# Kernel optimization log

Measured on AMD Instinct MI355X. Metric: run time of the kernel, lower is better.

## Reference

```python
import jax, jax.numpy as jnp
import numpy as np

B, C_IN, C_OUT, N, L = 4, 128, 256, 4096, 4
D = C_OUT // 4
EPS_BN = 1e-5


def setup_inputs() -> dict:
    key = jax.random.key(0)
    ks = jax.random.split(key, 16)
    s_in = 1.0 / np.sqrt(C_IN)
    s_out = 1.0 / np.sqrt(C_OUT)
    return {
        "features": jax.random.normal(ks[0], (B, C_IN, N), dtype=jnp.float32),
        # LBR: conv1x1 -> BN -> ReLU -> conv1x1 -> BN -> ReLU
        "lbr_w1": jax.random.uniform(ks[1], (C_OUT, C_IN), jnp.float32, -s_in, s_in),
        "lbr_g1": jnp.ones((C_OUT,), jnp.float32),
        "lbr_b1": jnp.zeros((C_OUT,), jnp.float32),
        "lbr_w2": jax.random.uniform(ks[2], (C_OUT, C_OUT), jnp.float32, -s_out, s_out),
        "lbr_g2": jnp.ones((C_OUT,), jnp.float32),
        "lbr_b2": jnp.zeros((C_OUT,), jnp.float32),
        # per-layer OffsetAttention params (stacked on leading L axis)
        # q_conv and k_conv share the same weight (q_conv.weight = k_conv.weight)
        "attn_qk_w": jax.random.uniform(ks[3], (L, D, C_OUT), jnp.float32, -s_out, s_out),
        "attn_v_w": jax.random.uniform(ks[4], (L, C_OUT, C_OUT), jnp.float32, -s_out, s_out),
        "attn_v_b": jax.random.uniform(ks[5], (L, C_OUT), jnp.float32, -s_out, s_out),
        "attn_t_w": jax.random.uniform(ks[6], (L, C_OUT, C_OUT), jnp.float32, -s_out, s_out),
        "attn_t_b": jax.random.uniform(ks[7], (L, C_OUT), jnp.float32, -s_out, s_out),
        "attn_bn_g": jnp.ones((L, C_OUT), jnp.float32),
        "attn_bn_b": jnp.zeros((L, C_OUT), jnp.float32),
    }


def batchnorm1d(x, gamma, beta):
    # x: [B, C, N]; training-mode BN: batch stats over (B, N), biased variance
    mean = jnp.mean(x, axis=(0, 2), keepdims=True)
    var = jnp.mean(jnp.square(x - mean), axis=(0, 2), keepdims=True)
    xn = (x - mean) * jax.lax.rsqrt(var + EPS_BN)
    return xn * gamma[None, :, None] + beta[None, :, None]


def offset_attention(x, qk_w, v_w, v_b, t_w, t_b, bn_g, bn_b):
    # x: [B, C, N]
    K = jnp.einsum("dc,bcn->bdn", qk_w, x)            # [B, D, N]
    # Q = same conv, permuted to [B, N, D]; attention_map = Q @ K -> [B, N, N]
    attn = jnp.einsum("bdn,bdm->bnm", K, K)
    attn = jax.nn.softmax(attn, axis=-1)
    # extra L1 renorm over dim=1 (column-wise)
    attn = attn / (1e-9 + jnp.sum(attn, axis=1, keepdims=True))
    V = jnp.einsum("dc,bcn->bdn", v_w, x) + v_b[None, :, None]  # [B, C, N]
    new_feat = jnp.einsum("bcn,bnm->bcm", V, attn)    # [B, C, N]
    off = x - new_feat
    t = jnp.einsum("dc,bcn->bdn", t_w, off) + t_b[None, :, None]
    return jax.nn.relu(batchnorm1d(t, bn_g, bn_b))


def reference(features, lbr_w1, lbr_g1, lbr_b1, lbr_w2, lbr_g2, lbr_b2,
              attn_qk_w, attn_v_w, attn_v_b, attn_t_w, attn_t_b,
              attn_bn_g, attn_bn_b):
    # LBR stem
    h = jnp.einsum("dc,bcn->bdn", lbr_w1, features)
    h = jax.nn.relu(batchnorm1d(h, lbr_g1, lbr_b1))
    h = jnp.einsum("dc,bcn->bdn", lbr_w2, h)
    h = jax.nn.relu(batchnorm1d(h, lbr_g2, lbr_b2))
    # stacked offset attention; output concatenates attention outputs only
    outs = []
    cur = h
    for i in range(L):
        cur = offset_attention(cur, attn_qk_w[i], attn_v_w[i], attn_v_b[i],
                               attn_t_w[i], attn_t_b[i], attn_bn_g[i], attn_bn_b[i])
        outs.append(cur)
    return jnp.concatenate(outs, axis=1)  # [B, C_OUT*L, N]
```

## Files before the change

### kernel.cpp

```cpp
#include <hip/hip_runtime.h>
#include <hip/hip_bf16.h>
#include <math.h>

#define NPTS 4096
#define CO   256
#define CI   128
#define BB   4
#define DQ   64
#define LL   4
#define PST  136

typedef __attribute__((ext_vector_type(8))) short bf16x8;
typedef __attribute__((ext_vector_type(4))) float f32x4;

#define MFMA16(a,b,c) __builtin_amdgcn_mfma_f32_16x16x32_bf16((a),(b),(c),0,0,0)

__device__ __forceinline__ short fb(float x) {
  __hip_bfloat16 h = __float2bfloat16(x);
  return __builtin_bit_cast(short, h);
}
__device__ __forceinline__ float bf(short s) {
  unsigned u = ((unsigned)(unsigned short)s) << 16;
  return __builtin_bit_cast(float, u);
}

__global__ __launch_bounds__(256) void cvt5_k(
    const float* __restrict__ s1, short* __restrict__ d1, int n1,
    const float* __restrict__ s2, short* __restrict__ d2, int n2,
    const float* __restrict__ s3, short* __restrict__ d3, int n3,
    const float* __restrict__ s4, short* __restrict__ d4, int n4,
    const float* __restrict__ s5, short* __restrict__ d5, int n5)
{
  int i = blockIdx.x * 256 + threadIdx.x;
  const float* S; short* D;
  if      (i < n1)                       { S = s1; D = d1; }
  else if ((i -= n1) < n2)               { S = s2; D = d2; }
  else if ((i -= n2) < n3)               { S = s3; D = d3; }
  else if ((i -= n3) < n4)               { S = s4; D = d4; }
  else if ((i -= n4) < n5)               { S = s5; D = d5; }
  else return;
  const float4 a = ((const float4*)S)[i * 2];
  const float4 b = ((const float4*)S)[i * 2 + 1];
  bf16x8 r;
  r[0] = fb(a.x); r[1] = fb(a.y); r[2] = fb(a.z); r[3] = fb(a.w);
  r[4] = fb(b.x); r[5] = fb(b.y); r[6] = fb(b.z); r[7] = fb(b.w);
  ((bf16x8*)D)[i] = r;
}

__global__ __launch_bounds__(256) void tcvt_k(
    const float* __restrict__ X, long xbs, int C, short* __restrict__ XT)
{
  const int n0 = blockIdx.x * 64, c0 = blockIdx.y * 64, b = blockIdx.z;
  const int t = threadIdx.x, tl = t & 63, tg = t >> 6;
  __shared__ float xs[64][65];
#pragma unroll
  for (int r = 0; r < 16; ++r) {
    const int cc = tg * 16 + r;
    xs[cc][tl] = X[(long)b * xbs + (long)(c0 + cc) * NPTS + n0 + tl];
  }
  __syncthreads();
#pragma unroll
  for (int r = 0; r < 16; ++r) {
    const int nn = tg * 16 + r;
    XT[((long)b * NPTS + n0 + nn) * C + c0 + tl] = fb(xs[tl][nn]);
  }
}

template<int OMODE, bool BIAS>
__global__ __launch_bounds__(256) void conv_a(
    const short* __restrict__ XT, int C,
    const short* __restrict__ Wb, const float* __restrict__ bias,
    short* __restrict__ Yv, long ybs,
    float* __restrict__ ps1, float* __restrict__ ps2)
{
  const int n0 = blockIdx.x * 64, d0 = blockIdx.y * 64, b = blockIdx.z;
  const int tid = threadIdx.x, w = tid >> 6, l = tid & 63, lg = l >> 4, lr = l & 15;
  const short* xb = XT + (long)b * NPTS * C;
  f32x4 acc[4];
#pragma unroll
  for (int i = 0; i < 4; ++i) acc[i] = (f32x4){0.f, 0.f, 0.f, 0.f};
  const int dr = d0 + w * 16 + lr;
  for (int kc = 0; kc < C; kc += 32) {
    const bf16x8 af = *(const bf16x8*)&Wb[(long)dr * C + kc + lg * 8];
#pragma unroll
    for (int ni = 0; ni < 4; ++ni) {
      const bf16x8 bx = *(const bf16x8*)&xb[(long)(n0 + ni * 16 + lr) * C + kc + lg * 8];
      acc[ni] = MFMA16(af, bx, acc[ni]);
    }
  }
  float bv[4] = {0.f, 0.f, 0.f, 0.f};
  if (BIAS) {
    const float4 b4 = *(const float4*)&bias[d0 + w * 16 + lg * 4];
    bv[0] = b4.x; bv[1] = b4.y; bv[2] = b4.z; bv[3] = b4.w;
  }
  const int db = d0 + w * 16 + lg * 4;
  float s1[4], s2[4];
#pragma unroll
  for (int j = 0; j < 4; ++j) { s1[j] = 0.f; s2[j] = 0.f; }
#pragma unroll
  for (int ni = 0; ni < 4; ++ni) {
    const int n = n0 + ni * 16 + lr;
#pragma unroll
    for (int j = 0; j < 4; ++j) {
      const short ob = fb(acc[ni][j] + bv[j]);
      if constexpr (OMODE == 1) {
        Yv[(long)b * ybs + ((long)(n >> 7) * CO + db + j) * 128 + (n & 127)] = ob;
      } else {
        Yv[(long)b * ybs + (long)(db + j) * NPTS + n] = ob;
        const float o = bf(ob);
        s1[j] += o; s2[j] += o * o;
      }
    }
  }
  if constexpr (OMODE == 2) {
#pragma unroll
    for (int j = 0; j < 4; ++j) {
#pragma unroll
      for (int off = 1; off < 16; off <<= 1) {
        s1[j] += __shfl_xor(s1[j], off);
        s2[j] += __shfl_xor(s2[j], off);
      }
    }
    if (lr == 0) {
      const int slot = b * 64 + blockIdx.x;
#pragma unroll
      for (int j = 0; j < 4; ++j) {
        ps1[(long)(db + j) * 256 + slot] = s1[j];
        ps2[(long)(db + j) * 256 + slot] = s2[j];
      }
    }
  }
}

__global__ __launch_bounds__(256) void conv_b(
    const short* __restrict__ XT, const short* __restrict__ Wb,
    short* __restrict__ KTo)
{
  const int n0 = blockIdx.x * 64, b = blockIdx.y;
  const int tid = threadIdx.x, w = tid >> 6, l = tid & 63, lg = l >> 4, lr = l & 15;
  const short* xb = XT + (long)b * NPTS * CO;
  f32x4 acc[4];
#pragma unroll
  for (int i = 0; i < 4; ++i) acc[i] = (f32x4){0.f, 0.f, 0.f, 0.f};
  const long nr = n0 + w * 16 + lr;
  for (int kc = 0; kc < CO; kc += 32) {
    const bf16x8 af = *(const bf16x8*)&xb[nr * CO + kc + lg * 8];
#pragma unroll
    for (int di = 0; di < 4; ++di) {
      const bf16x8 wf = *(const bf16x8*)&Wb[(long)(di * 16 + lr) * CO + kc + lg * 8];
      acc[di] = MFMA16(af, wf, acc[di]);
    }
  }
  short* Ko = KTo + (long)b * NPTS * DQ;
  const int nb = n0 + w * 16 + lg * 4;
#pragma unroll
  for (int j = 0; j < 4; ++j) {
#pragma unroll
    for (int di = 0; di < 4; ++di)
      Ko[(long)(nb + j) * DQ + di * 16 + lr] = fb(acc[di][j]);
  }
}

__global__ __launch_bounds__(64) void bnfin_k(
    const float* __restrict__ ps1, const float* __restrict__ ps2,
    float* __restrict__ mean, float* __restrict__ rstd)
{
  const int c = blockIdx.x, t = threadIdx.x;
  float s = 0.f, s2 = 0.f;
#pragma unroll
  for (int i = 0; i < 4; ++i) {
    s  += ps1[(long)c * 256 + t + i * 64];
    s2 += ps2[(long)c * 256 + t + i * 64];
  }
#pragma unroll
  for (int o = 32; o > 0; o >>= 1) { s += __shfl_down(s, o); s2 += __shfl_down(s2, o); }
  if (t == 0) {
    const float m = s / (float)(BB * NPTS);
    const float v = s2 / (float)(BB * NPTS) - m * m;
    mean[c] = m;
    rstd[c] = rsqrtf(v + 1e-5f);
  }
}

template<bool WF32, bool WBF>
__global__ __launch_bounds__(256) void bnrelu_t(
    const short* __restrict__ X, long xbs,
    const float* __restrict__ mean, const float* __restrict__ rstd,
    const float* __restrict__ g, const float* __restrict__ be,
    float* __restrict__ Yf, long ybs, short* __restrict__ XT)
{
  const int n0 = blockIdx.x * 64, c0 = blockIdx.y * 64, b = blockIdx.z;
  const int t = threadIdx.x, tl = t & 63, tg = t >> 6;
  __shared__ float xs[64][65];
#pragma unroll
  for (int r = 0; r < 16; ++r) {
    const int cc = tg * 16 + r, c = c0 + cc;
    float v = bf(X[(long)b * xbs + (long)c * NPTS + n0 + tl]);
    v = fmaxf((v - mean[c]) * rstd[c] * g[c] + be[c], 0.f);
    if (WF32) Yf[(long)b * ybs + (long)c * NPTS + n0 + tl] = v;
    xs[cc][tl] = v;
  }
  __syncthreads();
  if (WBF) {
#pragma unroll
    for (int r = 0; r < 16; ++r) {
      const int nn = tg * 16 + r;
      XT[((long)b * NPTS + n0 + nn) * CO + c0 + tl] = fb(xs[tl][nn]);
    }
  }
}

__global__ __launch_bounds__(256) void rowstats_mfma(
    const short* __restrict__ KT, float* __restrict__ pmax, float* __restrict__ psum)
{
  const int bid = blockIdx.x;
  const int b = (bid >> 1) & 3;
  const int idx = (bid >> 3) * 2 + (bid & 1);
  const int n0 = (idx & 63) * 64;
  const int chunk = idx >> 6;
  const int tid = threadIdx.x, w = tid >> 6, l = tid & 63, lg = l >> 4, lr = l & 15;
  const short* Kb = KT + (long)b * NPTS * DQ;
  const int nr = n0 + w * 16 + lr;
  const bf16x8 a0 = *(const bf16x8*)&Kb[(long)nr * DQ + lg * 8];
  const bf16x8 a1 = *(const bf16x8*)&Kb[(long)nr * DQ + 32 + lg * 8];
  const int mc = chunk * (NPTS / 4);

  float mx[4][4];
#pragma unroll
  for (int p = 0; p < 4; ++p)
#pragma unroll
    for (int j = 0; j < 4; ++j) mx[p][j] = -INFINITY;
  for (int m0 = mc; m0 < mc + NPTS / 4; m0 += 64) {
#pragma unroll
    for (int p = 0; p < 4; ++p) {
      const bf16x8 b0 = *(const bf16x8*)&Kb[(long)(m0 + p * 16 + lr) * DQ + lg * 8];
      const bf16x8 b1 = *(const bf16x8*)&Kb[(long)(m0 + p * 16 + lr) * DQ + 32 + lg * 8];
      f32x4 s = {0.f, 0.f, 0.f, 0.f};
      s = MFMA16(a0, b0, s);
      s = MFMA16(a1, b1, s);
#pragma unroll
      for (int j = 0; j < 4; ++j) mx[p][j] = fmaxf(mx[p][j], s[j]);
    }
  }
  float mxf[4];
#pragma unroll
  for (int j = 0; j < 4; ++j)
    mxf[j] = fmaxf(fmaxf(mx[0][j], mx[1][j]), fmaxf(mx[2][j], mx[3][j]));
#pragma unroll
  for (int off = 1; off < 16; off <<= 1)
#pragma unroll
    for (int j = 0; j < 4; ++j) mxf[j] = fmaxf(mxf[j], __shfl_xor(mxf[j], off));

  float sm[4] = {0.f, 0.f, 0.f, 0.f};
  for (int m0 = mc; m0 < mc + NPTS / 4; m0 += 64) {
#pragma unroll
    for (int p = 0; p < 4; ++p) {
      const bf16x8 b0 = *(const bf16x8*)&Kb[(long)(m0 + p * 16 + lr) * DQ + lg * 8];
      const bf16x8 b1 = *(const bf16x8*)&Kb[(long)(m0 + p * 16 + lr) * DQ + 32 + lg * 8];
      f32x4 s = {0.f, 0.f, 0.f, 0.f};
      s = MFMA16(a0, b0, s);
      s = MFMA16(a1, b1, s);
#pragma unroll
      for (int j = 0; j < 4; ++j) sm[j] += __expf(s[j] - mxf[j]);
    }
  }
#pragma unroll
  for (int off = 1; off < 16; off <<= 1)
#pragma unroll
    for (int j = 0; j < 4; ++j) sm[j] += __shfl_xor(sm[j], off);

  if (lr == 0) {
    const long base = ((long)chunk * BB + b) * NPTS + n0 + w * 16 + lg * 4;
#pragma unroll
    for (int j = 0; j < 4; ++j) { pmax[base + j] = mxf[j]; psum[base + j] = sm[j]; }
  }
}

__global__ __launch_bounds__(256) void combine_k(
    const float* __restrict__ pmax, const float* __restrict__ psum,
    float* __restrict__ rmax, float* __restrict__ rinv)
{
  const long i = (long)blockIdx.x * 256 + threadIdx.x;
  const long st = (long)BB * NPTS;
  float m = pmax[i];
  m = fmaxf(m, pmax[st + i]); m = fmaxf(m, pmax[2 * st + i]); m = fmaxf(m, pmax[3 * st + i]);
  const float s = psum[i] * __expf(pmax[i] - m)
                + psum[st + i] * __expf(pmax[st + i] - m)
                + psum[2 * st + i] * __expf(pmax[2 * st + i] - m)
                + psum[3 * st + i] * __expf(pmax[3 * st + i] - m);
  rmax[i] = m;
  rinv[i] = 1.f / s;
}

__global__ __launch_bounds__(512) void pass2_mfma(
    const short* __restrict__ KT, const short* __restrict__ Vblk,
    const float* __restrict__ rmax, const float* __restrict__ rinv,
    short* __restrict__ XO)
{
  const int bid = blockIdx.x;
  const int b  = (bid >> 1) & 3;
  const int m0 = ((bid >> 3) * 2 + (bid & 1)) * 64;
  const int tid = threadIdx.x;
  const int w = tid >> 6, l = tid & 63, lg = l >> 4, lr = l & 15;

  const short* Kb = KT + (long)b * NPTS * DQ;
  const short* Vb = Vblk + (long)b * CO * NPTS;
  const float* rmb = rmax + (long)b * NPTS;
  const float* rib = rinv + (long)b * NPTS;

  __shared__ short Ps[2][64][PST];
  __shared__ float cspart[8][64];
  __shared__ float csum[64];

  bf16x8 bK[4][2];
#pragma unroll
  for (int ms = 0; ms < 4; ++ms) {
    bK[ms][0] = *(const bf16x8*)&Kb[(long)(m0 + ms * 16 + lr) * DQ + lg * 8];
    bK[ms][1] = *(const bf16x8*)&Kb[(long)(m0 + ms * 16 + lr) * DQ + 32 + lg * 8];
  }

  f32x4 acc[4][2];
#pragma unroll
  for (int i = 0; i < 4; ++i) {
    acc[i][0] = (f32x4){0.f, 0.f, 0.f, 0.f};
    acc[i][1] = (f32x4){0.f, 0.f, 0.f, 0.f};
  }
  float cs[4] = {0.f, 0.f, 0.f, 0.f};
  const int c0 = w * 32;
  const int nb = w * 16;

  bf16x8 a0 = *(const bf16x8*)&Kb[(long)(nb + lr) * DQ + lg * 8];
  bf16x8 a1 = *(const bf16x8*)&Kb[(long)(nb + lr) * DQ + 32 + lg * 8];
  float4 rm4 = *(const float4*)&rmb[nb + lg * 4];
  float4 ri4 = *(const float4*)&rib[nb + lg * 4];

  int buf = 0;
  for (int n0 = 0; n0 < NPTS; n0 += 128) {
    const short* vt = Vb + (long)(n0 >> 7) * CO * 128;
    bf16x8 vf[4][2];
#pragma unroll
    for (int kc = 0; kc < 4; ++kc) {
      vf[kc][0] = *(const bf16x8*)&vt[(long)(c0 + lr) * 128 + kc * 32 + lg * 8];
      vf[kc][1] = *(const bf16x8*)&vt[(long)(c0 + 16 + lr) * 128 + kc * 32 + lg * 8];
    }
    f32x4 s[4];
#pragma unroll
    for (int ms = 0; ms < 4; ++ms) {
      s[ms] = (f32x4){0.f, 0.f, 0.f, 0.f};
      s[ms] = MFMA16(a0, bK[ms][0], s[ms]);
      s[ms] = MFMA16(a1, bK[ms][1], s[ms]);
    }
#pragma unroll
    for (int ms = 0; ms < 4; ++ms) {
      const float p0 = __expf(s[ms][0] - rm4.x) * ri4.x;
      const float p1 = __expf(s[ms][1] - rm4.y) * ri4.y;
      const float p2 = __expf(s[ms][2] - rm4.z) * ri4.z;
      const float p3 = __expf(s[ms][3] - rm4.w) * ri4.w;
      cs[ms] += p0 + p1 + p2 + p3;
      const unsigned u0 = ((unsigned)(unsigned short)fb(p1) << 16) | (unsigned short)fb(p0);
      const unsigned u1 = ((unsigned)(unsigned short)fb(p3) << 16) | (unsigned short)fb(p2);
      *(uint2*)&Ps[buf][ms * 16 + lr][nb + lg * 4] = make_uint2(u0, u1);
    }
    asm volatile("s_waitcnt lgkmcnt(0)" ::: "memory");
    __builtin_amdgcn_s_barrier();
    if (n0 + 128 < NPTS) {
      a0  = *(const bf16x8*)&Kb[(long)(n0 + 128 + nb + lr) * DQ + lg * 8];
      a1  = *(const bf16x8*)&Kb[(long)(n0 + 128 + nb + lr) * DQ + 32 + lg * 8];
      rm4 = *(const float4*)&rmb[n0 + 128 + nb + lg * 4];
      ri4 = *(const float4*)&rib[n0 + 128 + nb + lg * 4];
    }
#pragma unroll
    for (int kc = 0; kc < 4; ++kc) {
      bf16x8 pa[4];
#pragma unroll
      for (int ms = 0; ms < 4; ++ms)
        pa[ms] = *(const bf16x8*)&Ps[buf][ms * 16 + lr][kc * 32 + lg * 8];
#pragma unroll
      for (int ms = 0; ms < 4; ++ms) {
        acc[ms][0] = MFMA16(pa[ms], vf[kc][0], acc[ms][0]);
        acc[ms][1] = MFMA16(pa[ms], vf[kc][1], acc[ms][1]);
      }
    }
    buf ^= 1;
  }

  __syncthreads();
#pragma unroll
  for (int ms = 0; ms < 4; ++ms) {
    float csv = cs[ms];
    csv += __shfl_xor(csv, 16); csv += __shfl_xor(csv, 32);
    if (lg == 0) cspart[w][ms * 16 + lr] = csv;
  }
  __syncthreads();
  if (tid < 64) {
    float s = 0.f;
#pragma unroll
    for (int ww = 0; ww < 8; ++ww) s += cspart[ww][tid];
    csum[tid] = s;
  }
  __syncthreads();

  short* XOb = XO + (long)b * NPTS * CO;
#pragma unroll
  for (int ms = 0; ms < 4; ++ms) {
#pragma unroll
    for (int j = 0; j < 4; ++j) {
      const int m = m0 + ms * 16 + lg * 4 + j;
      const float inv = 1.f / (1e-9f + csum[ms * 16 + lg * 4 + j]);
      const long i0 = (long)m * CO + c0 + lr;
      const long i1 = (long)m * CO + c0 + 16 + lr;
      XOb[i0] = fb(bf(XOb[i0]) - acc[ms][0][j] * inv);
      XOb[i1] = fb(bf(XOb[i1]) - acc[ms][1][j] * inv);
    }
  }
}

extern "C" void kernel_launch(void* const* d_in, const int* in_sizes, int n_in,
                              void* d_out, int out_size, void* d_ws, size_t ws_size,
                              hipStream_t stream)
{
  const float* feat = (const float*)d_in[0];
  const float* w1   = (const float*)d_in[1];
  const float* g1   = (const float*)d_in[2];
  const float* b1   = (const float*)d_in[3];
  const float* w2   = (const float*)d_in[4];
  const float* g2   = (const float*)d_in[5];
  const float* b2   = (const float*)d_in[6];
  const float* qkw  = (const float*)d_in[7];
  const float* vw   = (const float*)d_in[8];
  const float* vb   = (const float*)d_in[9];
  const float* tw   = (const float*)d_in[10];
  const float* tb   = (const float*)d_in[11];
  const float* bng  = (const float*)d_in[12];
  const float* bnb  = (const float*)d_in[13];

  float* out = (float*)d_out;

  short* xt    = (short*)d_ws;
  short* KTb   = xt + (long)BB * NPTS * CO;
  short* Vblk  = KTb + (long)BB * NPTS * DQ;
  short* wb1   = Vblk + (long)BB * CO * NPTS;
  short* wb2   = wb1 + (long)CO * CI;
  short* wqk   = wb2 + (long)CO * CO;
  short* wv    = wqk + (long)LL * DQ * CO;
  short* wt    = wv + (long)LL * CO * CO;
  float* pmaxb = (float*)(wt + (long)LL * CO * CO);
  float* psumb = pmaxb + (long)4 * BB * NPTS;
  float* rmaxb = psumb + (long)4 * BB * NPTS;
  float* rinvb = rmaxb + (long)BB * NPTS;
  float* ps1   = rinvb + (long)BB * NPTS;
  float* ps2   = ps1 + (long)CO * 256;
  float* meanb = ps2 + (long)CO * 256;
  float* rstdb = meanb + CO;

  const long OBS = (long)LL * CO * NPTS;
  const long TBS = (long)CO * NPTS;
  short* pre = Vblk;

  const dim3 blk(256);

  {
    const int n1 = CO * CI / 8, n2 = CO * CO / 8, n3 = LL * DQ * CO / 8,
              n4 = LL * CO * CO / 8, n5 = LL * CO * CO / 8;
    const int tot = n1 + n2 + n3 + n4 + n5;
    cvt5_k<<<dim3((tot + 255) / 256), blk, 0, stream>>>(
        w1, wb1, n1, w2, wb2, n2, qkw, wqk, n3, vw, wv, n4, tw, wt, n5);
  }

  tcvt_k<<<dim3(64, 2, BB), blk, 0, stream>>>(feat, (long)CI * NPTS, CI, xt);
  conv_a<2, false><<<dim3(64, 4, BB), blk, 0, stream>>>(
      xt, CI, wb1, nullptr, pre, TBS, ps1, ps2);
  bnfin_k<<<dim3(CO), dim3(64), 0, stream>>>(ps1, ps2, meanb, rstdb);
  bnrelu_t<false, true><<<dim3(64, 4, BB), blk, 0, stream>>>(
      pre, TBS, meanb, rstdb, g1, b1, nullptr, 0, xt);
  conv_a<2, false><<<dim3(64, 4, BB), blk, 0, stream>>>(
      xt, CO, wb2, nullptr, pre, TBS, ps1, ps2);
  bnfin_k<<<dim3(CO), dim3(64), 0, stream>>>(ps1, ps2, meanb, rstdb);
  bnrelu_t<false, true><<<dim3(64, 4, BB), blk, 0, stream>>>(
      pre, TBS, meanb, rstdb, g2, b2, nullptr, 0, xt);

  for (int lyr = 0; lyr < LL; ++lyr) {
    float* nft = out + (long)lyr * CO * NPTS;
    conv_b<<<dim3(64, BB), blk, 0, stream>>>(xt, wqk + (long)lyr * DQ * CO, KTb);
    conv_a<1, true><<<dim3(64, 4, BB), blk, 0, stream>>>(
        xt, CO, wv + (long)lyr * CO * CO, vb + (long)lyr * CO, Vblk, TBS, nullptr, nullptr);
    rowstats_mfma<<<dim3(1024), blk, 0, stream>>>(KTb, pmaxb, psumb);
    combine_k<<<dim3(BB * NPTS / 256), blk, 0, stream>>>(pmaxb, psumb, rmaxb, rinvb);
    pass2_mfma<<<dim3(256), dim3(512), 0, stream>>>(KTb, Vblk, rmaxb, rinvb, xt);
    conv_a<2, true><<<dim3(64, 4, BB), blk, 0, stream>>>(
        xt, CO, wt + (long)lyr * CO * CO, tb + (long)lyr * CO, pre, TBS, ps1, ps2);
    bnfin_k<<<dim3(CO), dim3(64), 0, stream>>>(ps1, ps2, meanb, rstdb);
    if (lyr < LL - 1) {
      bnrelu_t<true, true><<<dim3(64, 4, BB), blk, 0, stream>>>(
          pre, TBS, meanb, rstdb, bng + (long)lyr * CO, bnb + (long)lyr * CO, nft, OBS, xt);
    } else {
      bnrelu_t<true, false><<<dim3(64, 4, BB), blk, 0, stream>>>(
          pre, TBS, meanb, rstdb, bng + (long)lyr * CO, bnb + (long)lyr * CO, nft, OBS, nullptr);
    }
  }
}
```

Measured before the change: 1.109 ms.

## Use online softmax in rowstats and split pass2 output channels across two blocks

rowstats_mfma now computes max and sum-of-exp in one pass with an online rescaling update, instead of running two passes that each recompute QK^T. The partials are merged with log-sum-exp-style shuffles. pass2_mfma splits the 256 output channels across two blocks, so the grid grows from 256 to 512 blocks and each block carries half the accumulators, with a min-blocks launch bound added. The cost is that each block recomputes the score tile and softmax exps twice over the whole grid, and rowstats runs an exp on every element plus extra selects.

```diff
diff --git a/kernel.cpp b/kernel.cpp
--- a/kernel.cpp
+++ b/kernel.cpp
@@ -223,13 +223,14 @@
   const int nr = n0 + w * 16 + lr;
   const bf16x8 a0 = *(const bf16x8*)&Kb[(long)nr * DQ + lg * 8];
   const bf16x8 a1 = *(const bf16x8*)&Kb[(long)nr * DQ + 32 + lg * 8];
+
+  float mx[4][4], sm[4][4];
+#pragma unroll
+  for (int p = 0; p < 4; ++p)
+#pragma unroll
+    for (int j = 0; j < 4; ++j) { mx[p][j] = -INFINITY; sm[p][j] = 0.f; }
+
   const int mc = chunk * (NPTS / 4);
-
-  float mx[4][4];
-#pragma unroll
-  for (int p = 0; p < 4; ++p)
-#pragma unroll
-    for (int j = 0; j < 4; ++j) mx[p][j] = -INFINITY;
   for (int m0 = mc; m0 < mc + NPTS / 4; m0 += 64) {
 #pragma unroll
     for (int p = 0; p < 4; ++p) {
@@ -239,40 +240,39 @@
       s = MFMA16(a0, b0, s);
       s = MFMA16(a1, b1, s);
 #pragma unroll
-      for (int j = 0; j < 4; ++j) mx[p][j] = fmaxf(mx[p][j], s[j]);
-    }
-  }
-  float mxf[4];
-#pragma unroll
-  for (int j = 0; j < 4; ++j)
-    mxf[j] = fmaxf(fmaxf(mx[0][j], mx[1][j]), fmaxf(mx[2][j], mx[3][j]));
-#pragma unroll
-  for (int off = 1; off < 16; off <<= 1)
-#pragma unroll
-    for (int j = 0; j < 4; ++j) mxf[j] = fmaxf(mxf[j], __shfl_xor(mxf[j], off));
-
-  float sm[4] = {0.f, 0.f, 0.f, 0.f};
-  for (int m0 = mc; m0 < mc + NPTS / 4; m0 += 64) {
-#pragma unroll
-    for (int p = 0; p < 4; ++p) {
-      const bf16x8 b0 = *(const bf16x8*)&Kb[(long)(m0 + p * 16 + lr) * DQ + lg * 8];
-      const bf16x8 b1 = *(const bf16x8*)&Kb[(long)(m0 + p * 16 + lr) * DQ + 32 + lg * 8];
-      f32x4 s = {0.f, 0.f, 0.f, 0.f};
-      s = MFMA16(a0, b0, s);
-      s = MFMA16(a1, b1, s);
-#pragma unroll
-      for (int j = 0; j < 4; ++j) sm[j] += __expf(s[j] - mxf[j]);
-    }
-  }
-#pragma unroll
-  for (int off = 1; off < 16; off <<= 1)
-#pragma unroll
-    for (int j = 0; j < 4; ++j) sm[j] += __shfl_xor(sm[j], off);
-
+      for (int j = 0; j < 4; ++j) {
+        const float d = s[j] - mx[p][j];
+        const float e = __expf(-fabsf(d));
+        const bool gt = d > 0.f;
+        sm[p][j] = gt ? fmaf(sm[p][j], e, 1.f) : (sm[p][j] + e);
+        mx[p][j] = gt ? s[j] : mx[p][j];
+      }
+    }
+  }
+#pragma unroll
+  for (int p = 1; p < 4; ++p)
+#pragma unroll
+    for (int j = 0; j < 4; ++j) {
+      const float m2 = fmaxf(mx[0][j], mx[p][j]);
+      sm[0][j] = sm[0][j] * __expf(mx[0][j] - m2) + sm[p][j] * __expf(mx[p][j] - m2);
+      mx[0][j] = m2;
+    }
+
+  float mx0 = mx[0][0], mx1 = mx[0][1], mx2 = mx[0][2], mx3 = mx[0][3];
+  float sm0 = sm[0][0], sm1 = sm[0][1], sm2 = sm[0][2], sm3 = sm[0][3];
+#define MRG(MX, SM, OFF) { const float om_ = __shfl_xor(MX, OFF); \
+  const float os_ = __shfl_xor(SM, OFF); \
+  const float m2_ = fmaxf(MX, om_); \
+  SM = SM * __expf(MX - m2_) + os_ * __expf(om_ - m2_); MX = m2_; }
+#pragma unroll
+  for (int off = 1; off < 16; off <<= 1) {
+    MRG(mx0, sm0, off); MRG(mx1, sm1, off);
+    MRG(mx2, sm2, off); MRG(mx3, sm3, off);
+  }
   if (lr == 0) {
     const long base = ((long)chunk * BB + b) * NPTS + n0 + w * 16 + lg * 4;
-#pragma unroll
-    for (int j = 0; j < 4; ++j) { pmax[base + j] = mxf[j]; psum[base + j] = sm[j]; }
+    pmax[base + 0] = mx0; pmax[base + 1] = mx1; pmax[base + 2] = mx2; pmax[base + 3] = mx3;
+    psum[base + 0] = sm0; psum[base + 1] = sm1; psum[base + 2] = sm2; psum[base + 3] = sm3;
   }
 }
 
@@ -292,14 +292,15 @@
   rinv[i] = 1.f / s;
 }
 
-__global__ __launch_bounds__(512) void pass2_mfma(
+__global__ __launch_bounds__(512, 4) void pass2_mfma(
     const short* __restrict__ KT, const short* __restrict__ Vblk,
     const float* __restrict__ rmax, const float* __restrict__ rinv,
     short* __restrict__ XO)
 {
   const int bid = blockIdx.x;
   const int b  = (bid >> 1) & 3;
-  const int m0 = ((bid >> 3) * 2 + (bid & 1)) * 64;
+  const int ch = bid & 1;
+  const int m0 = (bid >> 3) * 64;
   const int tid = threadIdx.x;
   const int w = tid >> 6, l = tid & 63, lg = l >> 4, lr = l & 15;
 
@@ -319,14 +320,11 @@
     bK[ms][1] = *(const bf16x8*)&Kb[(long)(m0 + ms * 16 + lr) * DQ + 32 + lg * 8];
   }
 
-  f32x4 acc[4][2];
-#pragma unroll
-  for (int i = 0; i < 4; ++i) {
-    acc[i][0] = (f32x4){0.f, 0.f, 0.f, 0.f};
-    acc[i][1] = (f32x4){0.f, 0.f, 0.f, 0.f};
-  }
+  f32x4 acc[4];
+#pragma unroll
+  for (int i = 0; i < 4; ++i) acc[i] = (f32x4){0.f, 0.f, 0.f, 0.f};
   float cs[4] = {0.f, 0.f, 0.f, 0.f};
-  const int c0 = w * 32;
+  const int c0 = ch * 128 + w * 16;
   const int nb = w * 16;
 
   bf16x8 a0 = *(const bf16x8*)&Kb[(long)(nb + lr) * DQ + lg * 8];
@@ -337,12 +335,10 @@
   int buf = 0;
   for (int n0 = 0; n0 < NPTS; n0 += 128) {
     const short* vt = Vb + (long)(n0 >> 7) * CO * 128;
-    bf16x8 vf[4][2];
-#pragma unroll
-    for (int kc = 0; kc < 4; ++kc) {
-      vf[kc][0] = *(const bf16x8*)&vt[(long)(c0 + lr) * 128 + kc * 32 + lg * 8];
-      vf[kc][1] = *(const bf16x8*)&vt[(long)(c0 + 16 + lr) * 128 + kc * 32 + lg * 8];
-    }
+    bf16x8 vf[4];
+#pragma unroll
+    for (int kc = 0; kc < 4; ++kc)
+      vf[kc] = *(const bf16x8*)&vt[(long)(c0 + lr) * 128 + kc * 32 + lg * 8];
     f32x4 s[4];
 #pragma unroll
     for (int ms = 0; ms < 4; ++ms) {
@@ -376,10 +372,8 @@
       for (int ms = 0; ms < 4; ++ms)
         pa[ms] = *(const bf16x8*)&Ps[buf][ms * 16 + lr][kc * 32 + lg * 8];
 #pragma unroll
-      for (int ms = 0; ms < 4; ++ms) {
-        acc[ms][0] = MFMA16(pa[ms], vf[kc][0], acc[ms][0]);
-        acc[ms][1] = MFMA16(pa[ms], vf[kc][1], acc[ms][1]);
-      }
+      for (int ms = 0; ms < 4; ++ms)
+        acc[ms] = MFMA16(pa[ms], vf[kc], acc[ms]);
     }
     buf ^= 1;
   }
@@ -408,9 +402,7 @@
       const int m = m0 + ms * 16 + lg * 4 + j;
       const float inv = 1.f / (1e-9f + csum[ms * 16 + lg * 4 + j]);
       const long i0 = (long)m * CO + c0 + lr;
-      const long i1 = (long)m * CO + c0 + 16 + lr;
-      XOb[i0] = fb(bf(XOb[i0]) - acc[ms][0][j] * inv);
-      XOb[i1] = fb(bf(XOb[i1]) - acc[ms][1][j] * inv);
+      XOb[i0] = fb(bf(XOb[i0]) - acc[ms][j] * inv);
     }
   }
 }
@@ -486,7 +478,7 @@
         xt, CO, wv + (long)lyr * CO * CO, vb + (long)lyr * CO, Vblk, TBS, nullptr, nullptr);
     rowstats_mfma<<<dim3(1024), blk, 0, stream>>>(KTb, pmaxb, psumb);
     combine_k<<<dim3(BB * NPTS / 256), blk, 0, stream>>>(pmaxb, psumb, rmaxb, rinvb);
-    pass2_mfma<<<dim3(256), dim3(512), 0, stream>>>(KTb, Vblk, rmaxb, rinvb, xt);
+    pass2_mfma<<<dim3(512), dim3(512), 0, stream>>>(KTb, Vblk, rmaxb, rinvb, xt);
     conv_a<2, true><<<dim3(64, 4, BB), blk, 0, stream>>>(
         xt, CO, wt + (long)lyr * CO * CO, tb + (long)lyr * CO, pre, TBS, ps1, ps2);
     bnfin_k<<<dim3(CO), dim3(64), 0, stream>>>(ps1, ps2, meanb, rstdb);
```

Result: faster. 978.9 us (-11.7%).

## Replace softmax row-max pass with Cauchy-Schwarz bound and halve pass2 tile

Applied to the files above, without the earlier changes.

conv_b now also computes each row's squared K norm, and a new bound_k kernel sets the per-row softmax shift to sqrt(|k_n|^2 * max|k_m|^2), an upper bound on every row logit. This removes the max-finding sweep over the N×N logits in the row-stats kernel and simplifies the partial-sum combine. pass2 also moves from 64-column to 32-column tiles, with twice as many blocks and a launch-bounds occupancy hint. The bound can sit well above the true row max, so exp terms may underflow and sums can lose accuracy when key norms vary widely.

```diff
diff --git a/kernel.cpp b/kernel.cpp
--- a/kernel.cpp
+++ b/kernel.cpp
@@ -134,7 +134,7 @@
 
 __global__ __launch_bounds__(256) void conv_b(
     const short* __restrict__ XT, const short* __restrict__ Wb,
-    short* __restrict__ KTo)
+    short* __restrict__ KTo, float* __restrict__ nrm2)
 {
   const int n0 = blockIdx.x * 64, b = blockIdx.y;
   const int tid = threadIdx.x, w = tid >> 6, l = tid & 63, lg = l >> 4, lr = l & 15;
@@ -153,12 +153,41 @@
   }
   short* Ko = KTo + (long)b * NPTS * DQ;
   const int nb = n0 + w * 16 + lg * 4;
+  float nv[4];
 #pragma unroll
   for (int j = 0; j < 4; ++j) {
-#pragma unroll
-    for (int di = 0; di < 4; ++di)
+    nv[j] = 0.f;
+#pragma unroll
+    for (int di = 0; di < 4; ++di) {
       Ko[(long)(nb + j) * DQ + di * 16 + lr] = fb(acc[di][j]);
-  }
+      nv[j] = fmaf(acc[di][j], acc[di][j], nv[j]);
+    }
+  }
+#pragma unroll
+  for (int j = 0; j < 4; ++j) {
+#pragma unroll
+    for (int off = 1; off < 16; off <<= 1) nv[j] += __shfl_xor(nv[j], off);
+  }
+  if (lr == 0) {
+#pragma unroll
+    for (int j = 0; j < 4; ++j) nrm2[(long)b * NPTS + nb + j] = nv[j];
+  }
+}
+
+__global__ __launch_bounds__(256) void bound_k(
+    const float* __restrict__ nrm2, float* __restrict__ rmax)
+{
+  const int b = blockIdx.x, t = threadIdx.x;
+  __shared__ float red[4];
+  float mx = 0.f;
+  for (int n = t; n < NPTS; n += 256) mx = fmaxf(mx, nrm2[(long)b * NPTS + n]);
+#pragma unroll
+  for (int o = 32; o > 0; o >>= 1) mx = fmaxf(mx, __shfl_down(mx, o));
+  if ((t & 63) == 0) red[t >> 6] = mx;
+  __syncthreads();
+  const float mv = fmaxf(fmaxf(red[0], red[1]), fmaxf(red[2], red[3]));
+  for (int n = t; n < NPTS; n += 256)
+    rmax[(long)b * NPTS + n] = sqrtf(nrm2[(long)b * NPTS + n] * mv);
 }
 
 __global__ __launch_bounds__(64) void bnfin_k(
@@ -210,8 +239,9 @@
   }
 }
 
-__global__ __launch_bounds__(256) void rowstats_mfma(
-    const short* __restrict__ KT, float* __restrict__ pmax, float* __restrict__ psum)
+__global__ __launch_bounds__(256) void rowsum_mfma(
+    const short* __restrict__ KT, const float* __restrict__ rmax,
+    float* __restrict__ psum)
 {
   const int bid = blockIdx.x;
   const int b = (bid >> 1) & 3;
@@ -223,13 +253,15 @@
   const int nr = n0 + w * 16 + lr;
   const bf16x8 a0 = *(const bf16x8*)&Kb[(long)nr * DQ + lg * 8];
   const bf16x8 a1 = *(const bf16x8*)&Kb[(long)nr * DQ + 32 + lg * 8];
+  const float4 M4 = *(const float4*)&rmax[(long)b * NPTS + n0 + w * 16 + lg * 4];
+
+  float sm[4][4];
+#pragma unroll
+  for (int p = 0; p < 4; ++p)
+#pragma unroll
+    for (int j = 0; j < 4; ++j) sm[p][j] = 0.f;
+
   const int mc = chunk * (NPTS / 4);
-
-  float mx[4][4];
-#pragma unroll
-  for (int p = 0; p < 4; ++p)
-#pragma unroll
-    for (int j = 0; j < 4; ++j) mx[p][j] = -INFINITY;
   for (int m0 = mc; m0 < mc + NPTS / 4; m0 += 64) {
 #pragma unroll
     for (int p = 0; p < 4; ++p) {
@@ -238,68 +270,44 @@
       f32x4 s = {0.f, 0.f, 0.f, 0.f};
       s = MFMA16(a0, b0, s);
       s = MFMA16(a1, b1, s);
-#pragma unroll
-      for (int j = 0; j < 4; ++j) mx[p][j] = fmaxf(mx[p][j], s[j]);
-    }
-  }
-  float mxf[4];
+      sm[p][0] += __expf(s[0] - M4.x);
+      sm[p][1] += __expf(s[1] - M4.y);
+      sm[p][2] += __expf(s[2] - M4.z);
+      sm[p][3] += __expf(s[3] - M4.w);
+    }
+  }
+  float sf[4];
 #pragma unroll
   for (int j = 0; j < 4; ++j)
-    mxf[j] = fmaxf(fmaxf(mx[0][j], mx[1][j]), fmaxf(mx[2][j], mx[3][j]));
+    sf[j] = (sm[0][j] + sm[1][j]) + (sm[2][j] + sm[3][j]);
 #pragma unroll
   for (int off = 1; off < 16; off <<= 1)
 #pragma unroll
-    for (int j = 0; j < 4; ++j) mxf[j] = fmaxf(mxf[j], __shfl_xor(mxf[j], off));
-
-  float sm[4] = {0.f, 0.f, 0.f, 0.f};
-  for (int m0 = mc; m0 < mc + NPTS / 4; m0 += 64) {
-#pragma unroll
-    for (int p = 0; p < 4; ++p) {
-      const bf16x8 b0 = *(const bf16x8*)&Kb[(long)(m0 + p * 16 + lr) * DQ + lg * 8];
-      const bf16x8 b1 = *(const bf16x8*)&Kb[(long)(m0 + p * 16 + lr) * DQ + 32 + lg * 8];
-      f32x4 s = {0.f, 0.f, 0.f, 0.f};
-      s = MFMA16(a0, b0, s);
-      s = MFMA16(a1, b1, s);
-#pragma unroll
-      for (int j = 0; j < 4; ++j) sm[j] += __expf(s[j] - mxf[j]);
-    }
-  }
-#pragma unroll
-  for (int off = 1; off < 16; off <<= 1)
-#pragma unroll
-    for (int j = 0; j < 4; ++j) sm[j] += __shfl_xor(sm[j], off);
+    for (int j = 0; j < 4; ++j) sf[j] += __shfl_xor(sf[j], off);
 
   if (lr == 0) {
     const long base = ((long)chunk * BB + b) * NPTS + n0 + w * 16 + lg * 4;
 #pragma unroll
-    for (int j = 0; j < 4; ++j) { pmax[base + j] = mxf[j]; psum[base + j] = sm[j]; }
-  }
-}
-
-__global__ __launch_bounds__(256) void combine_k(
-    const float* __restrict__ pmax, const float* __restrict__ psum,
-    float* __restrict__ rmax, float* __restrict__ rinv)
+    for (int j = 0; j < 4; ++j) psum[base + j] = sf[j];
+  }
+}
+
+__global__ __launch_bounds__(256) void combine_sum(
+    const float* __restrict__ psum, float* __restrict__ rinv)
 {
   const long i = (long)blockIdx.x * 256 + threadIdx.x;
   const long st = (long)BB * NPTS;
-  float m = pmax[i];
-  m = fmaxf(m, pmax[st + i]); m = fmaxf(m, pmax[2 * st + i]); m = fmaxf(m, pmax[3 * st + i]);
-  const float s = psum[i] * __expf(pmax[i] - m)
-                + psum[st + i] * __expf(pmax[st + i] - m)
-                + psum[2 * st + i] * __expf(pmax[2 * st + i] - m)
-                + psum[3 * st + i] * __expf(pmax[3 * st + i] - m);
-  rmax[i] = m;
-  rinv[i] = 1.f / s;
-}
-
-__global__ __launch_bounds__(512) void pass2_mfma(
+  rinv[i] = 1.f / ((psum[i] + psum[st + i]) + (psum[2 * st + i] + psum[3 * st + i]));
+}
+
+__global__ __launch_bounds__(512, 4) void pass2_mfma(
     const short* __restrict__ KT, const short* __restrict__ Vblk,
     const float* __restrict__ rmax, const float* __restrict__ rinv,
     short* __restrict__ XO)
 {
   const int bid = blockIdx.x;
   const int b  = (bid >> 1) & 3;
-  const int m0 = ((bid >> 3) * 2 + (bid & 1)) * 64;
+  const int m0 = ((bid >> 3) * 2 + (bid & 1)) * 32;
   const int tid = threadIdx.x;
   const int w = tid >> 6, l = tid & 63, lg = l >> 4, lr = l & 15;
 
@@ -308,24 +316,24 @@
   const float* rmb = rmax + (long)b * NPTS;
   const float* rib = rinv + (long)b * NPTS;
 
-  __shared__ short Ps[2][64][PST];
-  __shared__ float cspart[8][64];
-  __shared__ float csum[64];
-
-  bf16x8 bK[4][2];
-#pragma unroll
-  for (int ms = 0; ms < 4; ++ms) {
+  __shared__ short Ps[2][32][PST];
+  __shared__ float cspart[8][32];
+  __shared__ float csum[32];
+
+  bf16x8 bK[2][2];
+#pragma unroll
+  for (int ms = 0; ms < 2; ++ms) {
     bK[ms][0] = *(const bf16x8*)&Kb[(long)(m0 + ms * 16 + lr) * DQ + lg * 8];
     bK[ms][1] = *(const bf16x8*)&Kb[(long)(m0 + ms * 16 + lr) * DQ + 32 + lg * 8];
   }
 
-  f32x4 acc[4][2];
-#pragma unroll
-  for (int i = 0; i < 4; ++i) {
+  f32x4 acc[2][2];
+#pragma unroll
+  for (int i = 0; i < 2; ++i) {
     acc[i][0] = (f32x4){0.f, 0.f, 0.f, 0.f};
     acc[i][1] = (f32x4){0.f, 0.f, 0.f, 0.f};
   }
-  float cs[4] = {0.f, 0.f, 0.f, 0.f};
+  float cs[2] = {0.f, 0.f};
   const int c0 = w * 32;
   const int nb = w * 16;
 
@@ -343,15 +351,15 @@
       vf[kc][0] = *(const bf16x8*)&vt[(long)(c0 + lr) * 128 + kc * 32 + lg * 8];
       vf[kc][1] = *(const bf16x8*)&vt[(long)(c0 + 16 + lr) * 128 + kc * 32 + lg * 8];
     }
-    f32x4 s[4];
-#pragma unroll
-    for (int ms = 0; ms < 4; ++ms) {
+    f32x4 s[2];
+#pragma unroll
+    for (int ms = 0; ms < 2; ++ms) {
       s[ms] = (f32x4){0.f, 0.f, 0.f, 0.f};
       s[ms] = MFMA16(a0, bK[ms][0], s[ms]);
       s[ms] = MFMA16(a1, bK[ms][1], s[ms]);
     }
 #pragma unroll
-    for (int ms = 0; ms < 4; ++ms) {
+    for (int ms = 0; ms < 2; ++ms) {
       const float p0 = __expf(s[ms][0] - rm4.x) * ri4.x;
       const float p1 = __expf(s[ms][1] - rm4.y) * ri4.y;
       const float p2 = __expf(s[ms][2] - rm4.z) * ri4.z;
@@ -371,12 +379,12 @@
     }
 #pragma unroll
     for (int kc = 0; kc < 4; ++kc) {
-      bf16x8 pa[4];
-#pragma unroll
-      for (int ms = 0; ms < 4; ++ms)
+      bf16x8 pa[2];
+#pragma unroll
+      for (int ms = 0; ms < 2; ++ms)
         pa[ms] = *(const bf16x8*)&Ps[buf][ms * 16 + lr][kc * 32 + lg * 8];
 #pragma unroll
-      for (int ms = 0; ms < 4; ++ms) {
+      for (int ms = 0; ms < 2; ++ms) {
         acc[ms][0] = MFMA16(pa[ms], vf[kc][0], acc[ms][0]);
         acc[ms][1] = MFMA16(pa[ms], vf[kc][1], acc[ms][1]);
       }
@@ -386,13 +394,13 @@
 
   __syncthreads();
 #pragma unroll
-  for (int ms = 0; ms < 4; ++ms) {
+  for (int ms = 0; ms < 2; ++ms) {
     float csv = cs[ms];
     csv += __shfl_xor(csv, 16); csv += __shfl_xor(csv, 32);
     if (lg == 0) cspart[w][ms * 16 + lr] = csv;
   }
   __syncthreads();
-  if (tid < 64) {
+  if (tid < 32) {
     float s = 0.f;
 #pragma unroll
     for (int ww = 0; ww < 8; ++ww) s += cspart[ww][tid];
@@ -402,7 +410,7 @@
 
   short* XOb = XO + (long)b * NPTS * CO;
 #pragma unroll
-  for (int ms = 0; ms < 4; ++ms) {
+  for (int ms = 0; ms < 2; ++ms) {
 #pragma unroll
     for (int j = 0; j < 4; ++j) {
       const int m = m0 + ms * 16 + lg * 4 + j;
@@ -444,9 +452,9 @@
   short* wqk   = wb2 + (long)CO * CO;
   short* wv    = wqk + (long)LL * DQ * CO;
   short* wt    = wv + (long)LL * CO * CO;
-  float* pmaxb = (float*)(wt + (long)LL * CO * CO);
-  float* psumb = pmaxb + (long)4 * BB * NPTS;
-  float* rmaxb = psumb + (long)4 * BB * NPTS;
+  float* psumb = (float*)(wt + (long)LL * CO * CO);
+  float* nrm2b = psumb + (long)4 * BB * NPTS;
+  float* rmaxb = nrm2b + (long)BB * NPTS;
   float* rinvb = rmaxb + (long)BB * NPTS;
   float* ps1   = rinvb + (long)BB * NPTS;
   float* ps2   = ps1 + (long)CO * 256;
@@ -481,12 +489,13 @@
 
   for (int lyr = 0; lyr < LL; ++lyr) {
     float* nft = out + (long)lyr * CO * NPTS;
-    conv_b<<<dim3(64, BB), blk, 0, stream>>>(xt, wqk + (long)lyr * DQ * CO, KTb);
+    conv_b<<<dim3(64, BB), blk, 0, stream>>>(xt, wqk + (long)lyr * DQ * CO, KTb, nrm2b);
+    bound_k<<<dim3(BB), blk, 0, stream>>>(nrm2b, rmaxb);
     conv_a<1, true><<<dim3(64, 4, BB), blk, 0, stream>>>(
         xt, CO, wv + (long)lyr * CO * CO, vb + (long)lyr * CO, Vblk, TBS, nullptr, nullptr);
-    rowstats_mfma<<<dim3(1024), blk, 0, stream>>>(KTb, pmaxb, psumb);
-    combine_k<<<dim3(BB * NPTS / 256), blk, 0, stream>>>(pmaxb, psumb, rmaxb, rinvb);
-    pass2_mfma<<<dim3(256), dim3(512), 0, stream>>>(KTb, Vblk, rmaxb, rinvb, xt);
+    rowsum_mfma<<<dim3(1024), blk, 0, stream>>>(KTb, rmaxb, psumb);
+    combine_sum<<<dim3(BB * NPTS / 256), blk, 0, stream>>>(psumb, rinvb);
+    pass2_mfma<<<dim3(512), dim3(512), 0, stream>>>(KTb, Vblk, rmaxb, rinvb, xt);
     conv_a<2, true><<<dim3(64, 4, BB), blk, 0, stream>>>(
         xt, CO, wt + (long)lyr * CO * CO, tb + (long)lyr * CO, pre, TBS, ps1, ps2);
     bnfin_k<<<dim3(CO), dim3(64), 0, stream>>>(ps1, ps2, meanb, rstdb);
```

New measurement: 1.201 ms. 1.08x slower.
